# Optimization experiments

Hardware: AMD Instinct MI355X
Metric: run time of the kernel (lower is better)

The kernel has to match this reference:

```python
import jax, jax.numpy as jnp
import numpy as np
from functools import partial

P = 7          # cfg.POOLING_SIZE
SAMP = 2       # fixed sampling ratio (torchvision sampling_ratio=0 is adaptive; fixed 2 used for jit)
IM_H, IM_W = 800.0, 1216.0


def conv2d(x, w, b, pad):
    y = jax.lax.conv_general_dilated(
        x, w, window_strides=(1, 1), padding=[(pad, pad), (pad, pad)],
        dimension_numbers=("NCHW", "OIHW", "NCHW"))
    return y + b[None, :, None, None]


def upsample_add(x, y):
    # F.upsample(x, size=(H,W), mode='bilinear') + y  (align_corners=False / half-pixel)
    return jax.image.resize(x, y.shape, method="bilinear") + y


def roi_align_level(feat, rois, scale):
    """torchvision roi_align (aligned=False) of all rois on one feature map.
    feat: [B,C,H,W]; rois: [N,5] = (batch_idx, x1,y1,x2,y2) in image coords.
    Returns [N,C,P,P]."""
    B, C, H, W = feat.shape
    Hf, Wf = float(H), float(W)

    def one(roi):
        b = roi[0].astype(jnp.int32)
        img = jnp.take(feat, b, axis=0)                       # [C,H,W]
        x1, y1, x2, y2 = roi[1] * scale, roi[2] * scale, roi[3] * scale, roi[4] * scale
        rw = jnp.maximum(x2 - x1, 1.0)
        rh = jnp.maximum(y2 - y1, 1.0)
        bh, bw = rh / P, rw / P
        # sample coords per bin: [P, SAMP] -> flat [P*SAMP]
        ys = (y1 + jnp.arange(P, dtype=feat.dtype)[:, None] * bh
              + (jnp.arange(SAMP, dtype=feat.dtype)[None, :] + 0.5) * bh / SAMP).reshape(-1)
        xs = (x1 + jnp.arange(P, dtype=feat.dtype)[:, None] * bw
              + (jnp.arange(SAMP, dtype=feat.dtype)[None, :] + 0.5) * bw / SAMP).reshape(-1)
        vy = (ys >= -1.0) & (ys <= Hf)
        vx = (xs >= -1.0) & (xs <= Wf)
        yc = jnp.clip(ys, 0.0, Hf - 1.0)
        xc = jnp.clip(xs, 0.0, Wf - 1.0)
        y0 = jnp.floor(yc).astype(jnp.int32)
        x0 = jnp.floor(xc).astype(jnp.int32)
        y1i = jnp.minimum(y0 + 1, H - 1)
        x1i = jnp.minimum(x0 + 1, W - 1)
        ly = yc - y0.astype(feat.dtype)
        lx = xc - x0.astype(feat.dtype)
        hy, hx = 1.0 - ly, 1.0 - lx
        v00 = img[:, y0[:, None], x0[None, :]]                # [C, PS, PS]
        v01 = img[:, y0[:, None], x1i[None, :]]
        v10 = img[:, y1i[:, None], x0[None, :]]
        v11 = img[:, y1i[:, None], x1i[None, :]]
        val = (hy[:, None] * hx[None, :]) * v00 + (hy[:, None] * lx[None, :]) * v01 \
            + (ly[:, None] * hx[None, :]) * v10 + (ly[:, None] * lx[None, :]) * v11
        val = val * (vy[:, None] & vx[None, :]).astype(feat.dtype)
        return val.reshape(C, P, SAMP, P, SAMP).mean(axis=(2, 4))   # [C,P,P]

    return jax.vmap(one)(rois)


def setup_inputs() -> dict:
    key = jax.random.key(0)
    ks = jax.random.split(key, 24)
    B = 2
    c2 = jax.random.normal(ks[0], (B, 256, 200, 304), jnp.float32)
    c3 = jax.random.normal(ks[1], (B, 512, 100, 152), jnp.float32)
    c4 = jax.random.normal(ks[2], (B, 1024, 50, 76), jnp.float32)
    c5 = jax.random.normal(ks[3], (B, 2048, 25, 38), jnp.float32)
    # FPN params (all project to 256 channels)
    def w(k, o, i, s):
        return jax.random.normal(k, (o, i, s, s), jnp.float32) * 0.01
    w_top, b_top = w(ks[4], 256, 2048, 1), jnp.zeros((256,), jnp.float32)
    w_lat1, b_lat1 = w(ks[5], 256, 1024, 1), jnp.zeros((256,), jnp.float32)
    w_lat2, b_lat2 = w(ks[6], 256, 512, 1), jnp.zeros((256,), jnp.float32)
    w_lat3, b_lat3 = w(ks[7], 256, 256, 1), jnp.zeros((256,), jnp.float32)
    w_sm1, b_sm1 = w(ks[8], 256, 256, 3), jnp.zeros((256,), jnp.float32)
    w_sm2, b_sm2 = w(ks[9], 256, 256, 3), jnp.zeros((256,), jnp.float32)
    w_sm3, b_sm3 = w(ks[10], 256, 256, 3), jnp.zeros((256,), jnp.float32)
    # ROIs: batch idx + boxes with log-uniform sizes spanning pyramid levels 2..5
    N = 1024
    bidx = jax.random.randint(ks[11], (N,), 0, B).astype(jnp.float32)
    size = jnp.exp(jax.random.uniform(ks[12], (N,), jnp.float32,
                                      np.log(32.0), np.log(640.0)))
    ar = jnp.exp(jax.random.uniform(ks[13], (N,), jnp.float32,
                                    np.log(0.5), np.log(2.0)))
    bw_ = jnp.minimum(size * jnp.sqrt(ar), IM_W - 1)
    bh_ = jnp.minimum(size / jnp.sqrt(ar), IM_H - 1)
    x1 = jax.random.uniform(ks[14], (N,), jnp.float32) * (IM_W - bw_)
    y1 = jax.random.uniform(ks[15], (N,), jnp.float32) * (IM_H - bh_)
    rois = jnp.stack([bidx, x1, y1, x1 + bw_, y1 + bh_], axis=1)
    im_info = jnp.array([[IM_H, IM_W, 1.0]], jnp.float32)
    return dict(c2=c2, c3=c3, c4=c4, c5=c5, rois=rois, im_info=im_info,
                w_top=w_top, b_top=b_top, w_lat1=w_lat1, b_lat1=b_lat1,
                w_lat2=w_lat2, b_lat2=b_lat2, w_lat3=w_lat3, b_lat3=b_lat3,
                w_sm1=w_sm1, b_sm1=b_sm1, w_sm2=w_sm2, b_sm2=b_sm2,
                w_sm3=w_sm3, b_sm3=b_sm3)


def reference(c2, c3, c4, c5, rois, im_info,
              w_top, b_top, w_lat1, b_lat1, w_lat2, b_lat2, w_lat3, b_lat3,
              w_sm1, b_sm1, w_sm2, b_sm2, w_sm3, b_sm3):
    # --- FPN top-down pathway ---
    p5 = conv2d(c5, w_top, b_top, 0)
    p4 = conv2d(upsample_add(p5, conv2d(c4, w_lat1, b_lat1, 0)), w_sm1, b_sm1, 1)
    p3 = conv2d(upsample_add(p4, conv2d(c3, w_lat2, b_lat2, 0)), w_sm2, b_sm2, 1)
    p2 = conv2d(upsample_add(p3, conv2d(c2, w_lat3, b_lat3, 0)), w_sm3, b_sm3, 1)
    mrcnn_feats = [p2, p3, p4, p5]
    # --- _PyramidRoI_Feat (POOLING_MODE == 'align') ---
    h = rois[:, 4] - rois[:, 2] + 1.0
    w_ = rois[:, 3] - rois[:, 1] + 1.0
    lvl = jnp.round(jnp.log(jnp.sqrt(h * w_) / 224.0) + 4.0)
    lvl = jnp.clip(lvl, 2.0, 5.0)
    im_h = im_info[0, 0]
    N, C = rois.shape[0], p2.shape[1]
    out = jnp.zeros((N, C, P, P), p2.dtype)
    for i, l in enumerate(range(2, 6)):
        scale = mrcnn_feats[i].shape[2] / im_h
        feat_l = roi_align_level(mrcnn_feats[i], rois, scale)
        out = jnp.where((lvl == l)[:, None, None, None], feat_l, out)
    return out
```

## Files before the change

kernel.cpp:

```cpp
#include <hip/hip_runtime.h>
#include <math.h>

typedef __attribute__((ext_vector_type(8))) short short8;
typedef __attribute__((ext_vector_type(4))) float f32x4;
typedef __attribute__((ext_vector_type(8))) unsigned short ushort8v;

__device__ __forceinline__ ushort f2bf(float f) {
    unsigned u = __builtin_bit_cast(unsigned, f);
    u = (u + 0x7fffu + ((u >> 16) & 1u)) >> 16;
    return (ushort)u;
}
__device__ __forceinline__ float bf2f(ushort h) {
    unsigned u = ((unsigned)h) << 16;
    return __builtin_bit_cast(float, u);
}

__device__ __forceinline__ void cp16(const ushort* g, ushort* l) {
    __builtin_amdgcn_global_load_lds(
        (const __attribute__((address_space(1))) unsigned int*)g,
        (__attribute__((address_space(3))) unsigned int*)l, 16, 0, 0);
}

#define BARv(N) asm volatile("s_waitcnt vmcnt(" #N ") lgkmcnt(0)\n\ts_barrier" ::: "memory")

__device__ __forceinline__ void pair_decode(int bid, int nt, int& tile, int& mm) {
    int f16 = (nt * 2) & ~15;
    if (bid < f16) { tile = ((bid >> 4) << 3) | (bid & 7); mm = (bid >> 3) & 1; }
    else { int r = bid - f16; tile = (f16 >> 1) + (r >> 1); mm = r & 1; }
}


__global__ __launch_bounds__(256) void nchw2nhwc(const float* __restrict__ in,
                                                 ushort* __restrict__ out,
                                                 int C, int HW)
{
    __shared__ float tile[256][33];
    const int n  = blockIdx.z;
    const int c0 = blockIdx.y << 8;
    const int p0 = blockIdx.x << 5;
    const float* inp = in + (size_t)n * C * HW + (size_t)c0 * HW + p0;
    const int t = threadIdx.x;
    const int pr = t & 31, cr = t >> 5;
    const bool pok = (p0 + pr) < HW;
    #pragma unroll 8
    for (int i = 0; i < 32; ++i) {
        int c = i * 8 + cr;
        tile[c][pr] = pok ? inp[(size_t)c * HW + pr] : 0.f;
    }
    __syncthreads();
    ushort* op = out + (size_t)n * HW * C + c0;
    const int cp = (t & 127) * 2, ph = t >> 7;
    #pragma unroll 4
    for (int j = 0; j < 16; ++j) {
        int p = j * 2 + ph;
        if (p0 + p < HW) {
            ushort2 v;
            v.x = f2bf(tile[cp][p]);
            v.y = f2bf(tile[cp + 1][p]);
            *(ushort2*)&op[(size_t)(p0 + p) * C + cp] = v;
        }
    }
}

__global__ void cast_k(const float* __restrict__ in, ushort* __restrict__ out, int n)
{
    int i = blockIdx.x * 256 + threadIdx.x;
    if (i < n) out[i] = f2bf(in[i]);
}

__global__ void pack_w3(const float* __restrict__ w, ushort* __restrict__ wp, int Cin)
{
    int i = blockIdx.x * 256 + threadIdx.x;
    int total = 256 * Cin * 9;
    if (i >= total) return;
    int co  = i / (9 * Cin);
    int rem = i - co * 9 * Cin;
    int tap = rem / Cin;
    int ci  = rem - tap * Cin;
    wp[i] = f2bf(w[(size_t)co * Cin * 9 + (size_t)ci * 9 + tap]);
}

__global__ void zero_border(ushort* __restrict__ T, int Hp, int Wp, int NB, int total)
{
    int i = blockIdx.x * 256 + threadIdx.x;
    if (i >= total) return;
    const int cg = (i & 31) * 8;
    const int pb = i >> 5;
    const int n  = pb / NB;
    const int b  = pb - n * NB;
    int y, x;
    if (b < 2 * Wp) { y = (b < Wp) ? 0 : (Hp - 1); x = (b < Wp) ? b : (b - Wp); }
    else { int rem = b - 2 * Wp; y = 1 + (rem >> 1); x = (rem & 1) ? (Wp - 1) : 0; }
    ushort8v z = {0, 0, 0, 0, 0, 0, 0, 0};
    *(ushort8v*)&T[((size_t)n * Hp * Wp + (size_t)y * Wp + x) * 256 + cg] = z;
}

template<int PADOUT>
__global__ __launch_bounds__(256, 4) void conv1_mfma(
    const ushort* __restrict__ X, const ushort* __restrict__ Wt,
    const float* __restrict__ bias, ushort* __restrict__ Y,
    int Cin, int H, int Wd, int nP)
{
    const int HW = H * Wd;
    int tile, mm;
    pair_decode(blockIdx.x, nP, tile, mm);
    const int p0 = tile * 128;
    const int m0 = mm << 7;
    const int n  = blockIdx.z;
    const ushort* Xn = X + (size_t)n * HW * Cin;

    const int t    = threadIdx.x;
    const int lane = t & 63;
    const int wave = t >> 6;
    const int l15  = lane & 15, lq = lane >> 4;

    __shared__ __align__(16) ushort smem[17408];

    const int rA  = ((t >> 6) << 4) | (t & 15);
    const int lq8 = ((t >> 4) & 3) * 8;
    const ushort* agA = Wt + (size_t)(m0 + rA) * Cin + lq8;
    const ushort* agB = agA + (size_t)64 * Cin;
    const ushort* XqA = Xn + (size_t)(p0 + rA) * Cin + lq8;
    const ushort* XqB = Xn + (size_t)(p0 + rA + 64) * Cin + lq8;

    const int fr    = (lq * 16 + l15) * 8;
    const int aoff  = ((wave >> 1) * 4) * 512;
    const int boff  = 4096 + ((wave & 1) * 4) * 512;
    const int wbase = wave << 9;

    const int nch = Cin >> 5;

    auto stage = [&](int bb, int c) {
        const int kA = c << 5;
        cp16(agA + kA, &smem[bb + wbase]);
        cp16(agB + kA, &smem[bb + 2048 + wbase]);
        cp16(XqA + kA, &smem[bb + 4096 + wbase]);
        cp16(XqB + kA, &smem[bb + 6144 + wbase]);
    };

    f32x4 acc[4][4] = {};

    stage(0, 0);
    __syncthreads();

    #pragma unroll 1
    for (int c = 0; c < nch; c += 2) {
        {
            stage(8192, c + 1);
            short8 af[4], bf[4];
            #pragma unroll
            for (int mi = 0; mi < 4; ++mi) af[mi] = *(const short8*)&smem[aoff + mi * 512 + fr];
            #pragma unroll
            for (int ni = 0; ni < 4; ++ni) bf[ni] = *(const short8*)&smem[boff + ni * 512 + fr];
            #pragma unroll
            for (int mi = 0; mi < 4; ++mi)
                #pragma unroll
                for (int ni = 0; ni < 4; ++ni)
                    acc[mi][ni] = __builtin_amdgcn_mfma_f32_16x16x32_bf16(
                        af[mi], bf[ni], acc[mi][ni], 0, 0, 0);
            __syncthreads();
        }
        {
            if (c + 2 < nch) stage(0, c + 2);
            short8 af[4], bf[4];
            #pragma unroll
            for (int mi = 0; mi < 4; ++mi) af[mi] = *(const short8*)&smem[8192 + aoff + mi * 512 + fr];
            #pragma unroll
            for (int ni = 0; ni < 4; ++ni) bf[ni] = *(const short8*)&smem[8192 + boff + ni * 512 + fr];
            #pragma unroll
            for (int mi = 0; mi < 4; ++mi)
                #pragma unroll
                for (int ni = 0; ni < 4; ++ni)
                    acc[mi][ni] = __builtin_amdgcn_mfma_f32_16x16x32_bf16(
                        af[mi], bf[ni], acc[mi][ni], 0, 0, 0);
            __syncthreads();
        }
    }

    const int wm = (wave >> 1) * 64, wn = (wave & 1) * 64;
    #pragma unroll
    for (int mi = 0; mi < 4; ++mi) {
        const int co = wm + mi * 16 + lq * 4;
        float4 bv = *(const float4*)&bias[m0 + co];
        float bb4[4] = {bv.x, bv.y, bv.z, bv.w};
        #pragma unroll
        for (int ni = 0; ni < 4; ++ni) {
            const int p = wn + ni * 16 + l15;
            ushort4 h;
            h.x = f2bf(acc[mi][ni][0] + bb4[0]);
            h.y = f2bf(acc[mi][ni][1] + bb4[1]);
            h.z = f2bf(acc[mi][ni][2] + bb4[2]);
            h.w = f2bf(acc[mi][ni][3] + bb4[3]);
            *(ushort4*)&smem[p * 136 + co] = h;
        }
    }
    __syncthreads();

    ushort* Yn = PADOUT ? (Y + (size_t)n * (H + 2) * (Wd + 2) * 256)
                        : (Y + (size_t)n * HW * 256);
    #pragma unroll
    for (int it = 0; it < 8; ++it) {
        int idx = it * 256 + t;
        int px  = idx >> 4;
        int off = (idx & 15) * 8;
        int qq  = p0 + px;
        if (qq >= HW) continue;
        uint4 v = *(const uint4*)&smem[px * 136 + off];
        if (PADOUT) {
            int y = qq / Wd, x = qq - (qq / Wd) * Wd;
            *(uint4*)&Yn[((size_t)(y + 1) * (Wd + 2) + (x + 1)) * 256 + m0 + off] = v;
        } else {
            *(uint4*)&Yn[(size_t)qq * 256 + m0 + off] = v;
        }
    }
}

__global__ __launch_bounds__(256, 3) void conv3_mfma(
    const ushort* __restrict__ X, const ushort* __restrict__ Wt,
    const float* __restrict__ bias, ushort* __restrict__ Y,
    int Hout, int Wout, int ct, int nt)
{
    const int Wp = Wout + 2;
    int tile, mm;
    pair_decode(blockIdx.x, nt, tile, mm);
    const int ty = tile / ct, tx = tile - ty * ct;
    int y0 = ty * 8;  if (y0 > Hout - 8)  y0 = Hout - 8;
    int x0 = tx * 16; if (x0 > Wout - 16) x0 = Wout - 16;
    const int m0 = mm << 7;
    const int nb = blockIdx.z;
    const ushort* Xn = X + (size_t)nb * (Hout + 2) * Wp * 256;

    const int t    = threadIdx.x;
    const int lane = t & 63;
    const int wave = t >> 6;
    const int l15  = lane & 15, lq = lane >> 4;

    __shared__ __align__(16) ushort smem[23808];

    const int rSw = ((t >> 6) << 4) | ((t & 15) ^ (((t >> 4) & 3) << 1));
    const int lq8 = ((t >> 4) & 3) * 8;
    const ushort* agA = Wt + (size_t)(m0 + rSw) * 2304 + lq8;
    const ushort* agB = agA + (size_t)64 * 2304;

    const int fra  = (lq * 16 + (l15 ^ (lq << 1))) * 8;
    const int aoff = (wave >> 1) * 2048;
    const int bb   = (((wave & 1) * 16 + lq) * 144) + l15 * 8;

    auto stageA = [&](int ring, int ccA, int tapA) {
        const int kA = tapA * 256 + (ccA << 5);
        cp16(agA + kA, &smem[ring * 4096 + t * 8]);
        cp16(agB + kA, &smem[ring * 4096 + 2048 + t * 8]);
    };
    auto stageBr = [&](int bsel, int cc, int rnd) {
        const int cb = cc << 5;
        int s = rnd * 256 + t;
        if (s < 720) {
            int py  = s / 72, rem = s - py * 72;
            int lqq = rem / 18, pxc = rem - lqq * 18;
            cp16(Xn + ((size_t)(y0 + py) * Wp + (x0 + pxc)) * 256 + cb + lqq * 8,
                 &smem[12288 + bsel * 5760 + s * 8]);
        }
    };

    f32x4 acc[4][4] = {};

#define FRAG_MFMA(RING, BSEL, DY, DX)                                             \
    {                                                                             \
        short8 af[4], bf[4];                                                      \
        _Pragma("unroll")                                                         \
        for (int mi = 0; mi < 4; ++mi)                                            \
            af[mi] = *(const short8*)&smem[(RING) * 4096 + aoff + mi * 512 + fra];\
        _Pragma("unroll")                                                         \
        for (int ni = 0; ni < 4; ++ni)                                            \
            bf[ni] = *(const short8*)&smem[12288 + (BSEL) * 5760 + bb             \
                                           + (ni + (DY)) * 576 + (DX) * 8];       \
        __builtin_amdgcn_s_setprio(1);                                            \
        _Pragma("unroll")                                                         \
        for (int mi = 0; mi < 4; ++mi)                                            \
            _Pragma("unroll")                                                     \
            for (int ni = 0; ni < 4; ++ni)                                        \
                acc[mi][ni] = __builtin_amdgcn_mfma_f32_16x16x32_bf16(            \
                    af[mi], bf[ni], acc[mi][ni], 0, 0, 0);                        \
        __builtin_amdgcn_s_setprio(0);                                            \
    }

    stageBr(0, 0, 0); stageBr(0, 0, 1); stageBr(0, 0, 2);
    stageA(0, 0, 0);
    stageA(1, 0, 1);
    __syncthreads();

    #pragma unroll 1
    for (int cc = 0; cc < 8; ++cc) {
        const int bsel = cc & 1;
        const int ccn  = (cc < 7) ? cc + 1 : 7;
        stageA(2, cc, 2);                           FRAG_MFMA(0, bsel, 0, 0); BARv(2);
        stageA(0, cc, 3); stageBr(bsel ^ 1, ccn, 0); FRAG_MFMA(1, bsel, 0, 1); BARv(3);
        stageA(1, cc, 4); stageBr(bsel ^ 1, ccn, 1); FRAG_MFMA(2, bsel, 0, 2); BARv(3);
        stageA(2, cc, 5); stageBr(bsel ^ 1, ccn, 2); FRAG_MFMA(0, bsel, 1, 0); BARv(3);
        stageA(0, cc, 6);                           FRAG_MFMA(1, bsel, 1, 1); BARv(2);
        stageA(1, cc, 7);                           FRAG_MFMA(2, bsel, 1, 2); BARv(2);
        stageA(2, cc, 8);                           FRAG_MFMA(0, bsel, 2, 0); BARv(2);
        stageA(0, ccn, 0);                          FRAG_MFMA(1, bsel, 2, 1); BARv(2);
        stageA(1, ccn, 1);                          FRAG_MFMA(2, bsel, 2, 2); BARv(2);
    }
#undef FRAG_MFMA
    __syncthreads();

    const int wm = (wave >> 1) * 64, wn = (wave & 1) * 64;
    #pragma unroll
    for (int mi = 0; mi < 4; ++mi) {
        const int co = wm + mi * 16 + lq * 4;
        float4 bv = *(const float4*)&bias[m0 + co];
        float bb4[4] = {bv.x, bv.y, bv.z, bv.w};
        #pragma unroll
        for (int ni = 0; ni < 4; ++ni) {
            const int p = wn + ni * 16 + l15;
            ushort4 h;
            h.x = f2bf(acc[mi][ni][0] + bb4[0]);
            h.y = f2bf(acc[mi][ni][1] + bb4[1]);
            h.z = f2bf(acc[mi][ni][2] + bb4[2]);
            h.w = f2bf(acc[mi][ni][3] + bb4[3]);
            *(ushort4*)&smem[p * 136 + co] = h;
        }
    }
    __syncthreads();

    ushort* Yn = Y + (size_t)nb * Hout * Wout * 256;
    #pragma unroll
    for (int it = 0; it < 8; ++it) {
        int idx = it * 256 + t;
        int p   = idx >> 4;
        int off = (idx & 15) * 8;
        int yy  = y0 + (p >> 4), xx = x0 + (p & 15);
        *(uint4*)&Yn[((size_t)yy * Wout + xx) * 256 + m0 + off] =
            *(const uint4*)&smem[p * 136 + off];
    }
}

__global__ void upsample_add_nhwc(ushort* __restrict__ T, const ushort* __restrict__ Pn,
                                  int H, int Wd, int total32)
{
    int i = blockIdx.x * 256 + threadIdx.x;
    if (i >= total32) return;
    const int cg = (i & 31) * 8;
    const int q  = i >> 5;
    const int HW = H * Wd;
    const int n   = q / HW;
    const int pix = q - n * HW;
    const int y = pix / Wd, x = pix - (pix / Wd) * Wd;
    const int Hh = H >> 1, Wh = Wd >> 1;

    float sy = fminf(fmaxf(y * 0.5f - 0.25f, 0.f), (float)(Hh - 1));
    float sx = fminf(fmaxf(x * 0.5f - 0.25f, 0.f), (float)(Wh - 1));
    int y0 = (int)sy, x0 = (int)sx;
    int y1 = min(y0 + 1, Hh - 1), x1 = min(x0 + 1, Wh - 1);
    float fy = sy - (float)y0, fx = sx - (float)x0;

    const ushort* base = Pn + (size_t)n * Hh * Wh * 256 + cg;
    ushort8v a00 = *(const ushort8v*)&base[(size_t)(y0 * Wh + x0) * 256];
    ushort8v a01 = *(const ushort8v*)&base[(size_t)(y0 * Wh + x1) * 256];
    ushort8v a10 = *(const ushort8v*)&base[(size_t)(y1 * Wh + x0) * 256];
    ushort8v a11 = *(const ushort8v*)&base[(size_t)(y1 * Wh + x1) * 256];

    const int Wp2 = Wd + 2;
    ushort* tp = T + ((size_t)n * (H + 2) * Wp2 + (size_t)(y + 1) * Wp2 + (x + 1)) * 256 + cg;
    ushort8v tv = *(ushort8v*)tp;
    ushort8v r;
    #pragma unroll
    for (int j = 0; j < 8; ++j) {
        float v = (1.f - fy) * ((1.f - fx) * bf2f(a00[j]) + fx * bf2f(a01[j]))
                +        fy  * ((1.f - fx) * bf2f(a10[j]) + fx * bf2f(a11[j]));
        r[j] = f2bf(bf2f(tv[j]) + v);
    }
    *(ushort8v*)tp = r;
}

__global__ __launch_bounds__(256) void roi_align_k(
    const float* __restrict__ rois, const float* __restrict__ im_info,
    const ushort* __restrict__ p2, const ushort* __restrict__ p3,
    const ushort* __restrict__ p4, const ushort* __restrict__ p5,
    float* __restrict__ out)
{
    const int r   = blockIdx.x;
    const int tid = threadIdx.x;

    __shared__ int   s_y0[14], s_y1[14], s_x0[14], s_x1[14];
    __shared__ float s_ly[14], s_lx[14], s_vy[14], s_vx[14];
    __shared__ float s_o[256 * 49];

    const float bx  = rois[r * 5 + 0];
    const float x1r = rois[r * 5 + 1];
    const float y1r = rois[r * 5 + 2];
    const float x2r = rois[r * 5 + 3];
    const float y2r = rois[r * 5 + 4];

    const float hh = y2r - y1r + 1.f;
    const float ww = x2r - x1r + 1.f;
    float lf = rintf(logf(sqrtf(hh * ww) * (1.f / 224.f)) + 4.f);
    lf = fminf(fmaxf(lf, 2.f), 5.f);
    const int lvl = (int)lf;

    const ushort* feat; int H, W;
    if      (lvl == 2) { feat = p2; H = 200; W = 304; }
    else if (lvl == 3) { feat = p3; H = 100; W = 152; }
    else if (lvl == 4) { feat = p4; H = 50;  W = 76;  }
    else               { feat = p5; H = 25;  W = 38;  }

    const float im_h  = im_info[0];
    const float scale = (float)H / im_h;
    const float x1 = x1r * scale, y1 = y1r * scale;
    const float x2 = x2r * scale, y2 = y2r * scale;
    const float rw = fmaxf(x2 - x1, 1.f);
    const float rh = fmaxf(y2 - y1, 1.f);
    const float bh = rh * (1.f / 7.f);
    const float bw = rw * (1.f / 7.f);

    if (tid < 28) {
        if (tid < 14) {
            int i = tid, pi = i >> 1, s = i & 1;
            float ys = y1 + pi * bh + (s + 0.5f) * bh * 0.5f;
            float v  = (ys >= -1.f && ys <= (float)H) ? 1.f : 0.f;
            float yc = fminf(fmaxf(ys, 0.f), (float)H - 1.f);
            int y0 = (int)floorf(yc);
            s_y0[i] = y0; s_y1[i] = min(y0 + 1, H - 1);
            s_ly[i] = yc - (float)y0; s_vy[i] = v;
        } else {
            int i = tid - 14, pi = i >> 1, s = i & 1;
            float xs = x1 + pi * bw + (s + 0.5f) * bw * 0.5f;
            float v  = (xs >= -1.f && xs <= (float)W) ? 1.f : 0.f;
            float xc = fminf(fmaxf(xs, 0.f), (float)W - 1.f);
            int x0 = (int)floorf(xc);
            s_x0[i] = x0; s_x1[i] = min(x0 + 1, W - 1);
            s_lx[i] = xc - (float)x0; s_vx[i] = v;
        }
    }
    __syncthreads();

    const int b = (int)bx;
    const ushort* fc = feat + (size_t)b * H * W * 256 + tid;

    #pragma unroll
    for (int py = 0; py < 7; ++py) {
        #pragma unroll
        for (int px = 0; px < 7; ++px) {
            float acc = 0.f;
            #pragma unroll
            for (int sy = 0; sy < 2; ++sy) {
                #pragma unroll
                for (int sx = 0; sx < 2; ++sx) {
                    int iy = py * 2 + sy, ix = px * 2 + sx;
                    float ly = s_ly[iy], lx = s_lx[ix];
                    float hy = 1.f - ly, hx = 1.f - lx;
                    int y0 = s_y0[iy], y1i = s_y1[iy];
                    int x0 = s_x0[ix], x1i = s_x1[ix];
                    float v00 = bf2f(fc[(size_t)(y0 * W + x0) * 256]);
                    float v01 = bf2f(fc[(size_t)(y0 * W + x1i) * 256]);
                    float v10 = bf2f(fc[(size_t)(y1i * W + x0) * 256]);
                    float v11 = bf2f(fc[(size_t)(y1i * W + x1i) * 256]);
                    float val = hy * hx * v00 + hy * lx * v01
                              + ly * hx * v10 + ly * lx * v11;
                    acc += val * s_vy[iy] * s_vx[ix];
                }
            }
            s_o[tid * 49 + py * 7 + px] = acc * 0.25f;
        }
    }
    __syncthreads();
    float* orow = out + (size_t)r * 256 * 49;
    for (int it = 0; it < 49; ++it)
        orow[it * 256 + tid] = s_o[it * 256 + tid];
}

static inline int cdiv(int a, int b) { return (a + b - 1) / b; }

extern "C" void kernel_launch(void* const* d_in, const int* in_sizes, int n_in,
                              void* d_out, int out_size, void* d_ws, size_t ws_size,
                              hipStream_t stream) {
    const float* c2      = (const float*)d_in[0];
    const float* c3      = (const float*)d_in[1];
    const float* c4      = (const float*)d_in[2];
    const float* c5      = (const float*)d_in[3];
    const float* rois    = (const float*)d_in[4];
    const float* im_info = (const float*)d_in[5];
    const float* w_top   = (const float*)d_in[6];
    const float* b_top   = (const float*)d_in[7];
    const float* w_lat1  = (const float*)d_in[8];
    const float* b_lat1  = (const float*)d_in[9];
    const float* w_lat2  = (const float*)d_in[10];
    const float* b_lat2  = (const float*)d_in[11];
    const float* w_lat3  = (const float*)d_in[12];
    const float* b_lat3  = (const float*)d_in[13];
    const float* w_sm1   = (const float*)d_in[14];
    const float* b_sm1   = (const float*)d_in[15];
    const float* w_sm2   = (const float*)d_in[16];
    const float* b_sm2   = (const float*)d_in[17];
    const float* w_sm3   = (const float*)d_in[18];
    const float* b_sm3   = (const float*)d_in[19];
    float* out = (float*)d_out;
    ushort* ws = (ushort*)d_ws;

    ushort* c2t = ws;
    ushort* c3t = c2t + 31129600;
    ushort* c4t = c3t + 15564800;
    ushort* c5t = c4t + 7782400;
    ushort* p5  = c5t + 3891200;
    ushort* p4  = p5  + 486400;
    ushort* p3  = p4  + 1945600;
    ushort* T   = p3  + 7782400;
    ushort* wtp = T   + 31647744;
    ushort* wl1 = wtp + 524288;
    ushort* wl2 = wl1 + 262144;
    ushort* wl3 = wl2 + 131072;
    ushort* ws1 = wl3 + 65536;
    ushort* ws2 = ws1 + 589824;
    ushort* ws3 = ws2 + 589824;
    ushort* p2  = c2t;

    dim3 blk(256);

    cast_k<<<cdiv(524288, 256), blk, 0, stream>>>(w_top,  wtp, 524288);
    cast_k<<<cdiv(262144, 256), blk, 0, stream>>>(w_lat1, wl1, 262144);
    cast_k<<<cdiv(131072, 256), blk, 0, stream>>>(w_lat2, wl2, 131072);
    cast_k<<<cdiv(65536,  256), blk, 0, stream>>>(w_lat3, wl3, 65536);
    pack_w3<<<cdiv(589824, 256), blk, 0, stream>>>(w_sm1, ws1, 256);
    pack_w3<<<cdiv(589824, 256), blk, 0, stream>>>(w_sm2, ws2, 256);
    pack_w3<<<cdiv(589824, 256), blk, 0, stream>>>(w_sm3, ws3, 256);

    nchw2nhwc<<<dim3(1900, 1, 2), blk, 0, stream>>>(c2, c2t, 256,  60800);
    nchw2nhwc<<<dim3(475,  2, 2), blk, 0, stream>>>(c3, c3t, 512,  15200);
    nchw2nhwc<<<dim3(119,  4, 2), blk, 0, stream>>>(c4, c4t, 1024, 3800);
    nchw2nhwc<<<dim3(30,   8, 2), blk, 0, stream>>>(c5, c5t, 2048, 950);

    conv1_mfma<0><<<dim3(16, 1, 2), blk, 0, stream>>>(c5t, wtp, b_top, p5, 2048, 25, 38, 8);

    conv1_mfma<1><<<dim3(60, 1, 2), blk, 0, stream>>>(c4t, wl1, b_lat1, T, 1024, 50, 76, 30);
    zero_border<<<cdiv(16384, 256), blk, 0, stream>>>(T, 52, 78, 256, 16384);
    upsample_add_nhwc<<<cdiv(2 * 3800 * 32, 256), blk, 0, stream>>>(T, p5, 50, 76, 2 * 3800 * 32);
    conv3_mfma<<<dim3(70, 1, 2), blk, 0, stream>>>(T, ws1, b_sm1, p4, 50, 76, 5, 35);

    conv1_mfma<1><<<dim3(238, 1, 2), blk, 0, stream>>>(c3t, wl2, b_lat2, T, 512, 100, 152, 119);
    zero_border<<<cdiv(32512, 256), blk, 0, stream>>>(T, 102, 154, 508, 32512);
    upsample_add_nhwc<<<cdiv(2 * 15200 * 32, 256), blk, 0, stream>>>(T, p4, 100, 152, 2 * 15200 * 32);
    conv3_mfma<<<dim3(260, 1, 2), blk, 0, stream>>>(T, ws2, b_sm2, p3, 100, 152, 10, 130);

    conv1_mfma<1><<<dim3(950, 1, 2), blk, 0, stream>>>(c2t, wl3, b_lat3, T, 256, 200, 304, 475);
    zero_border<<<cdiv(64768, 256), blk, 0, stream>>>(T, 202, 306, 1012, 64768);
    upsample_add_nhwc<<<cdiv(2 * 60800 * 32, 256), blk, 0, stream>>>(T, p3, 200, 304, 2 * 60800 * 32);
    conv3_mfma<<<dim3(950, 1, 2), blk, 0, stream>>>(T, ws3, b_sm3, p2, 200, 304, 19, 475);

    roi_align_k<<<dim3(1024), blk, 0, stream>>>(rois, im_info, p2, p3, p4, p5, out);
}
```

Before: 1.052 ms.

## Double-buffer MFMA fragments in registers and drop LDS swizzle in 3x3 conv

Restructures the 3x3 conv main loop so the LDS fragment loads for the next tap go into a second register set while MFMAs run on the current set. This hides LDS read latency behind matrix math. The loop is unrolled over pairs of channel chunks, and the A-stage prologue is shifted by one tap. It also removes the XOR swizzle on the A-tile rows, which may bring back LDS bank conflicts, and the extra fragment registers raise register pressure.

```diff
diff --git a/kernel.cpp b/kernel.cpp
--- a/kernel.cpp
+++ b/kernel.cpp
@@ -237,12 +237,12 @@
 
     __shared__ __align__(16) ushort smem[23808];
 
-    const int rSw = ((t >> 6) << 4) | ((t & 15) ^ (((t >> 4) & 3) << 1));
+    const int rA  = ((t >> 6) << 4) | (t & 15);
     const int lq8 = ((t >> 4) & 3) * 8;
-    const ushort* agA = Wt + (size_t)(m0 + rSw) * 2304 + lq8;
+    const ushort* agA = Wt + (size_t)(m0 + rA) * 2304 + lq8;
     const ushort* agB = agA + (size_t)64 * 2304;
 
-    const int fra  = (lq * 16 + (l15 ^ (lq << 1))) * 8;
+    const int fra  = (lq * 16 + l15) * 8;
     const int aoff = (wave >> 1) * 2048;
     const int bb   = (((wave & 1) * 16 + lq) * 144) + l15 * 8;
 
@@ -263,47 +263,56 @@
     };
 
     f32x4 acc[4][4] = {};
-
-#define FRAG_MFMA(RING, BSEL, DY, DX)                                             \
+    short8 af0[4], bf0[4], af1[4], bf1[4];
+
+#define PREFETCH(S, RING, BSEL, DY, DX)                                           \
     {                                                                             \
-        short8 af[4], bf[4];                                                      \
         _Pragma("unroll")                                                         \
         for (int mi = 0; mi < 4; ++mi)                                            \
-            af[mi] = *(const short8*)&smem[(RING) * 4096 + aoff + mi * 512 + fra];\
+            af##S[mi] = *(const short8*)&smem[(RING) * 4096 + aoff + mi * 512 + fra];\
         _Pragma("unroll")                                                         \
         for (int ni = 0; ni < 4; ++ni)                                            \
-            bf[ni] = *(const short8*)&smem[12288 + (BSEL) * 5760 + bb             \
-                                           + (ni + (DY)) * 576 + (DX) * 8];       \
-        __builtin_amdgcn_s_setprio(1);                                            \
+            bf##S[ni] = *(const short8*)&smem[12288 + (BSEL) * 5760 + bb          \
+                                              + (ni + (DY)) * 576 + (DX) * 8];    \
+    }
+#define MFMA16(S)                                                                 \
+    __builtin_amdgcn_s_setprio(1);                                                \
+    _Pragma("unroll")                                                             \
+    for (int mi = 0; mi < 4; ++mi)                                                \
         _Pragma("unroll")                                                         \
-        for (int mi = 0; mi < 4; ++mi)                                            \
-            _Pragma("unroll")                                                     \
-            for (int ni = 0; ni < 4; ++ni)                                        \
-                acc[mi][ni] = __builtin_amdgcn_mfma_f32_16x16x32_bf16(            \
-                    af[mi], bf[ni], acc[mi][ni], 0, 0, 0);                        \
-        __builtin_amdgcn_s_setprio(0);                                            \
-    }
+        for (int ni = 0; ni < 4; ++ni)                                            \
+            acc[mi][ni] = __builtin_amdgcn_mfma_f32_16x16x32_bf16(                \
+                af##S[mi], bf##S[ni], acc[mi][ni], 0, 0, 0);                      \
+    __builtin_amdgcn_s_setprio(0);
+
+#define CHUNK(cc, ccn, CB, NB, E, O)                                               \
+    stageA(0, cc, 3);                             PREFETCH(O, 1, CB, 0, 1); MFMA16(E); BARv(2); \
+    stageA(1, cc, 4); stageBr(NB, ccn, 0);        PREFETCH(E, 2, CB, 0, 2); MFMA16(O); BARv(3); \
+    stageA(2, cc, 5); stageBr(NB, ccn, 1);        PREFETCH(O, 0, CB, 1, 0); MFMA16(E); BARv(3); \
+    stageA(0, cc, 6); stageBr(NB, ccn, 2);        PREFETCH(E, 1, CB, 1, 1); MFMA16(O); BARv(3); \
+    stageA(1, cc, 7);                             PREFETCH(O, 2, CB, 1, 2); MFMA16(E); BARv(2); \
+    stageA(2, cc, 8);                             PREFETCH(E, 0, CB, 2, 0); MFMA16(O); BARv(2); \
+    stageA(0, ccn, 0);                            PREFETCH(O, 1, CB, 2, 1); MFMA16(E); BARv(2); \
+    stageA(1, ccn, 1);                            PREFETCH(E, 2, CB, 2, 2); MFMA16(O); BARv(2); \
+    stageA(2, ccn, 2);                            PREFETCH(O, 0, NB, 0, 0); MFMA16(E); BARv(2);
 
     stageBr(0, 0, 0); stageBr(0, 0, 1); stageBr(0, 0, 2);
     stageA(0, 0, 0);
     stageA(1, 0, 1);
-    __syncthreads();
+    stageA(2, 0, 2);
+    __syncthreads();
+    PREFETCH(0, 0, 0, 0, 0);
 
     #pragma unroll 1
-    for (int cc = 0; cc < 8; ++cc) {
-        const int bsel = cc & 1;
-        const int ccn  = (cc < 7) ? cc + 1 : 7;
-        stageA(2, cc, 2);                           FRAG_MFMA(0, bsel, 0, 0); BARv(2);
-        stageA(0, cc, 3); stageBr(bsel ^ 1, ccn, 0); FRAG_MFMA(1, bsel, 0, 1); BARv(3);
-        stageA(1, cc, 4); stageBr(bsel ^ 1, ccn, 1); FRAG_MFMA(2, bsel, 0, 2); BARv(3);
-        stageA(2, cc, 5); stageBr(bsel ^ 1, ccn, 2); FRAG_MFMA(0, bsel, 1, 0); BARv(3);
-        stageA(0, cc, 6);                           FRAG_MFMA(1, bsel, 1, 1); BARv(2);
-        stageA(1, cc, 7);                           FRAG_MFMA(2, bsel, 1, 2); BARv(2);
-        stageA(2, cc, 8);                           FRAG_MFMA(0, bsel, 2, 0); BARv(2);
-        stageA(0, ccn, 0);                          FRAG_MFMA(1, bsel, 2, 1); BARv(2);
-        stageA(1, ccn, 1);                          FRAG_MFMA(2, bsel, 2, 2); BARv(2);
-    }
-#undef FRAG_MFMA
+    for (int cp = 0; cp < 4; ++cp) {
+        const int cc = 2 * cp, c1 = 2 * cp + 1;
+        const int c2 = (cp < 3) ? 2 * cp + 2 : 7;
+        CHUNK(cc, c1, 0, 1, 0, 1);
+        CHUNK(c1, c2, 1, 0, 1, 0);
+    }
+#undef CHUNK
+#undef MFMA16
+#undef PREFETCH
     __syncthreads();
 
     const int wm = (wave >> 1) * 64, wn = (wave & 1) * 64;
```

Result: slower. 1.165 ms (+10.7%).
